# Kernel optimization log

Measured on AMD Instinct MI355X. Metric: run time of the kernel, lower is better.

The kernel has to match this reference:

```python
import jax, jax.numpy as jnp
import numpy as np

DIM = 2048
NUM_HEADS = 16
NUM_KV_HEADS = 4
HEAD_DIM = DIM // NUM_HEADS
GROUP = NUM_HEADS // NUM_KV_HEADS
ROPE_THETA = 10000.0
EPS = 1e-6


def setup_inputs() -> dict:
    key = jax.random.key(0)
    ks = jax.random.split(key, 6)
    B, L = 2, 2048
    x = jax.random.normal(ks[0], (B, L, DIM), dtype=jnp.float32)
    mask = jnp.ones((B, L), dtype=jnp.int32)
    s = 1.0 / np.sqrt(DIM)
    Wq = jax.random.normal(ks[1], (DIM, DIM), dtype=jnp.float32) * s
    Wk = jax.random.normal(ks[2], (NUM_KV_HEADS * HEAD_DIM, DIM), dtype=jnp.float32) * s
    Wv = jax.random.normal(ks[3], (NUM_KV_HEADS * HEAD_DIM, DIM), dtype=jnp.float32) * s
    Wo = jax.random.normal(ks[4], (DIM, DIM), dtype=jnp.float32) * s
    q_gamma = jnp.ones((HEAD_DIM,), dtype=jnp.float32)
    k_gamma = jnp.ones((HEAD_DIM,), dtype=jnp.float32)
    return {"x": x, "mask": mask, "Wq": Wq, "Wk": Wk, "Wv": Wv, "Wo": Wo,
            "q_gamma": q_gamma, "k_gamma": k_gamma}


def _rmsnorm(x, gamma):
    # normalize over last dim (head_dim)
    var = jnp.mean(jnp.square(x), axis=-1, keepdims=True)
    return x * jax.lax.rsqrt(var + EPS) * gamma


def _rope_cos_sin(L):
    inv_freq = 1.0 / (ROPE_THETA ** (jnp.arange(0, HEAD_DIM, 2, dtype=jnp.float32) / HEAD_DIM))
    t = jnp.arange(L, dtype=jnp.float32)
    freqs = jnp.outer(t, inv_freq)  # [L, hd/2]
    return jnp.cos(freqs), jnp.sin(freqs)


def _apply_rotary(x, cos, sin):
    # x: [B, H, L, hd]; rotate consecutive pairs (complex mul)
    xr = x.reshape(*x.shape[:-1], HEAD_DIM // 2, 2)
    re, im = xr[..., 0], xr[..., 1]
    c = cos[None, None, :, :]
    s = sin[None, None, :, :]
    out_re = re * c - im * s
    out_im = re * s + im * c
    return jnp.stack([out_re, out_im], axis=-1).reshape(x.shape)


def reference(x, mask, Wq, Wk, Wv, Wo, q_gamma, k_gamma):
    B, L, D = x.shape
    q = (x @ Wq.T).reshape(B, L, NUM_HEADS, HEAD_DIM)
    k = (x @ Wk.T).reshape(B, L, NUM_KV_HEADS, HEAD_DIM)
    v = (x @ Wv.T).reshape(B, L, NUM_KV_HEADS, HEAD_DIM)
    q = _rmsnorm(q, q_gamma)
    k = _rmsnorm(k, k_gamma)
    q = q.transpose(0, 2, 1, 3)  # [B, H, L, hd]
    k = k.transpose(0, 2, 1, 3)  # [B, Hkv, L, hd]
    v = v.transpose(0, 2, 1, 3)
    cos, sin = _rope_cos_sin(L)
    q = _apply_rotary(q, cos, sin)
    k = _apply_rotary(k, cos, sin)
    # repeat_interleave kv heads to match query heads
    k = jnp.repeat(k, GROUP, axis=1)
    v = jnp.repeat(v, GROUP, axis=1)
    scores = jnp.einsum('bhqd,bhkd->bhqk', q, k) / jnp.sqrt(jnp.float32(HEAD_DIM))
    m = mask[:, None, None, :]  # [B,1,1,L] padding mask
    scores = jnp.where(m == 0, -jnp.inf, scores)
    attn = jax.nn.softmax(scores.astype(jnp.float32), axis=-1).astype(scores.dtype)
    out = jnp.einsum('bhqk,bhkd->bhqd', attn, v)
    out = out.transpose(0, 2, 1, 3).reshape(B, L, NUM_HEADS * HEAD_DIM)
    return out @ Wo.T
```

## Files before the change

### kernel.cpp

```cpp
#include <hip/hip_runtime.h>
#include <hip/hip_bf16.h>
#include <stdint.h>

#define DIMN   2048
#define L_SEQ  2048
#define BATCH  2
#define NHEADS 16
#define NKVH   4
#define HDIM   128
#define MROWS  (BATCH * L_SEQ)
#define NQKV   (DIMN + 2 * NKVH * HDIM)

typedef unsigned short u16;
typedef __bf16 bf16_t;
typedef bf16_t bf16x8 __attribute__((ext_vector_type(8)));
typedef float  f32x4  __attribute__((ext_vector_type(4)));
typedef float  f32x16 __attribute__((ext_vector_type(16)));
typedef u16    u16x8  __attribute__((ext_vector_type(8)));

__device__ __forceinline__ u16 f2bf(float f) {
  union { float f; uint32_t u; } v; v.f = f;
  uint32_t r = v.u + 0x7fffu + ((v.u >> 16) & 1u);
  return (u16)(r >> 16);
}

__device__ __forceinline__ float fexp2(float x) {
  float r; asm("v_exp_f32 %0, %1" : "=v"(r) : "v"(x)); return r;
}
__device__ __forceinline__ uint32_t cvtpk(float a, float b) {
  uint32_t r; asm("v_cvt_pk_bf16_f32 %0, %1, %2" : "=v"(r) : "v"(a), "v"(b)); return r;
}
__device__ __forceinline__ void plswap(uint32_t& a, uint32_t& b) {
  asm volatile("v_permlane32_swap_b32 %0, %1" : "+v"(a), "+v"(b));
}

#define GLOAD_LDS16(gp, lp)                                                     \
  __builtin_amdgcn_global_load_lds(                                             \
      (const __attribute__((address_space(1))) void*)(gp),                      \
      (__attribute__((address_space(3))) void*)(lp), 16, 0, 0)

__global__ void conv_f32_bf16(const float* __restrict__ src,
                              u16* __restrict__ dst, int n4) {
  int i = blockIdx.x * blockDim.x + threadIdx.x;
  int stride = gridDim.x * blockDim.x;
  for (; i < n4; i += stride) {
    float4 v = ((const float4*)src)[i];
    ushort4 o;
    o.x = f2bf(v.x); o.y = f2bf(v.y); o.z = f2bf(v.z); o.w = f2bf(v.w);
    ((ushort4*)dst)[i] = o;
  }
}

__global__ __launch_bounds__(256) void gemm_bf16_bt(
    const u16* __restrict__ A, const u16* __restrict__ B,
    float* __restrict__ C, int M, int N, int K) {
  __shared__ u16 As[128 * 64];
  __shared__ u16 Bs[128 * 64];
  const int tid  = threadIdx.x;
  const int lane = tid & 63;
  const int wid  = tid >> 6;
  const int l15  = lane & 15, l4 = lane >> 4;
  const int bm = blockIdx.y, bn = blockIdx.x;
  const int wr = wid >> 1, wc = wid & 1;

  f32x4 acc[4][4] = {};

  for (int k0 = 0; k0 < K; k0 += 64) {
#pragma unroll
    for (int is = 0; is < 4; ++is) {
      int cc = is * 256 + tid;
      int rr = cc >> 3, c = (cc & 7) << 3;
      GLOAD_LDS16(A + (size_t)(bm * 128 + rr) * K + k0 + c,
                  &As[(is * 256 + wid * 64) * 8]);
      GLOAD_LDS16(B + (size_t)(bn * 128 + rr) * K + k0 + c,
                  &Bs[(is * 256 + wid * 64) * 8]);
    }
    __syncthreads();

#pragma unroll
    for (int kk = 0; kk < 2; ++kk) {
      const int ko = kk * 32 + l4 * 8;
      bf16x8 af[4], bfr[4];
#pragma unroll
      for (int m = 0; m < 4; ++m)
        af[m] = *(const bf16x8*)&As[(wr * 64 + m * 16 + l15) * 64 + ko];
#pragma unroll
      for (int n = 0; n < 4; ++n)
        bfr[n] = *(const bf16x8*)&Bs[(wc * 64 + n * 16 + l15) * 64 + ko];
#pragma unroll
      for (int m = 0; m < 4; ++m)
#pragma unroll
        for (int n = 0; n < 4; ++n)
          acc[m][n] = __builtin_amdgcn_mfma_f32_16x16x32_bf16(
              af[m], bfr[n], acc[m][n], 0, 0, 0);
    }
    __syncthreads();
  }

  const int crow0 = bm * 128 + wr * 64;
  const int ccol0 = bn * 128 + wc * 64;
#pragma unroll
  for (int m = 0; m < 4; ++m)
#pragma unroll
    for (int n = 0; n < 4; ++n)
#pragma unroll
      for (int j = 0; j < 4; ++j)
        C[(size_t)(crow0 + m * 16 + l4 * 4 + j) * N + ccol0 + n * 16 + l15] =
            acc[m][n][j];
}

#define QK_PRE 0.12751743f
__global__ __launch_bounds__(256) void rms_rope(
    const float* __restrict__ qkv, const float* __restrict__ qg,
    const float* __restrict__ kg, u16* __restrict__ qb,
    u16* __restrict__ kb) {
  const int gw   = blockIdx.x * 4 + (threadIdx.x >> 6);
  const int lane = threadIdx.x & 63;
  const int row  = gw / 20;
  const int slot = gw % 20;
  const int b = row >> 11, pos = row & 2047;

  int colbase = (slot < 16) ? slot * 128 : 2048 + (slot - 16) * 128;
  const float* src = qkv + (size_t)row * NQKV + colbase;
  float2 v = *(const float2*)(src + 2 * lane);
  float re = v.x, im = v.y;

  float ss = re * re + im * im;
#pragma unroll
  for (int m = 1; m < 64; m <<= 1) ss += __shfl_xor(ss, m, 64);
  float inv = rsqrtf(ss * (1.0f / 128.0f) + 1e-6f);
  const float* gamma = (slot < 16) ? qg : kg;
  re = re * inv * gamma[2 * lane];
  im = im * inv * gamma[2 * lane + 1];
  float freq = fexp2(-(float)lane * (13.287712379549449f / 64.0f));
  float ang = (float)pos * freq;
  float s, c;
  sincosf(ang, &s, &c);
  float ore = re * c - im * s;
  float oim = re * s + im * c;
  if (slot < 16) { ore *= QK_PRE; oim *= QK_PRE; }

  ushort2 o; o.x = f2bf(ore); o.y = f2bf(oim);
  u16* dst = (slot < 16)
      ? qb + ((size_t)((b * NHEADS + slot) * L_SEQ) + pos) * HDIM + 2 * lane
      : kb + ((size_t)((b * NKVH + slot - 16) * L_SEQ) + pos) * HDIM + 2 * lane;
  *(ushort2*)dst = o;
}

__global__ __launch_bounds__(256) void transpose_v(
    const float* __restrict__ qkv, u16* __restrict__ vt) {
  __shared__ u16 Ls[64][68];
  const int pt = blockIdx.x;
  const int dt = blockIdx.y;
  const int b  = blockIdx.z;
  const int t  = threadIdx.x;
  {
    int r0 = t >> 4;
    int c4 = (t & 15) << 2;
#pragma unroll
    for (int i = 0; i < 4; ++i) {
      int row = i * 16 + r0;
      float4 v = *(const float4*)(qkv + (size_t)(b * 2048 + pt * 64 + row) * NQKV
                                  + 2560 + dt * 64 + c4);
      Ls[row][c4 + 0] = f2bf(v.x); Ls[row][c4 + 1] = f2bf(v.y);
      Ls[row][c4 + 2] = f2bf(v.z); Ls[row][c4 + 3] = f2bf(v.w);
    }
  }
  __syncthreads();
#pragma unroll
  for (int it = 0; it < 2; ++it) {
    int slot = it * 256 + t;
    int dr = slot >> 3, ch = slot & 7;
    u16x8 o;
#pragma unroll
    for (int j = 0; j < 8; ++j) o[j] = Ls[ch * 8 + j][dr];
    int vc = dt * 64 + dr;
    int kvh = vc >> 7, dd = vc & 127;
    *(u16x8*)(vt + ((size_t)(b * NKVH + kvh) * HDIM + dd) * L_SEQ + pt * 64 + ch * 8) = o;
  }
}

__global__ __launch_bounds__(512) void attn_kernel(
    const u16* __restrict__ qb, const u16* __restrict__ kb,
    const u16* __restrict__ vt, const int* __restrict__ mask,
    u16* __restrict__ ob) {
  __shared__ u16 Ks[2][64 * 128];
  __shared__ u16 Vs[2][128 * 64];

  const int tid = threadIdx.x;
  const int lane = tid & 63, wid = tid >> 6;
  const int l31 = lane & 31, hi = lane >> 5;
  const int qt = blockIdx.x;
  const int bh = blockIdx.y;
  const int b = bh >> 4, h = bh & 15, kvh = h >> 2;

  const u16* Q  = qb + ((size_t)((b * NHEADS + h) * L_SEQ) + qt * 256 + wid * 32) * HDIM;
  const u16* Kg = kb + (size_t)((b * NKVH + kvh) * L_SEQ) * HDIM;
  const u16* Vg = vt + (size_t)((b * NKVH + kvh) * HDIM) * L_SEQ;
  const int* msk = mask + b * L_SEQ;

  bf16x8 qf[8];
  {
    const u16* qrow = Q + l31 * HDIM + hi * 8;
#pragma unroll
    for (int ds = 0; ds < 8; ++ds) qf[ds] = *(const bf16x8*)(qrow + ds * 16);
  }

  f32x16 o[4] = {};
  float m_run = -1e30f, l_run = 0.f;

#define STAGE(buf, tt)                                                          \
  {                                                                             \
    const int kv0 = (tt) * 64;                                                  \
    _Pragma("unroll")                                                           \
    for (int it = 0; it < 2; ++it) {                                            \
      int cc = it * 512 + tid;                                                  \
      int kr = cc >> 4, cs = cc & 15;                                           \
      GLOAD_LDS16(Kg + (size_t)(kv0 + kr) * HDIM + ((cs ^ (kr & 7)) << 3),      \
                  &Ks[buf][(it * 512 + wid * 64) * 8]);                         \
    }                                                                           \
    _Pragma("unroll")                                                           \
    for (int it = 0; it < 2; ++it) {                                            \
      int cc = it * 512 + tid;                                                  \
      int dr = cc >> 3, cs = cc & 7;                                            \
      GLOAD_LDS16(Vg + (size_t)dr * L_SEQ + kv0 + ((cs ^ (dr & 7)) << 3),       \
                  &Vs[buf][(it * 512 + wid * 64) * 8]);                         \
    }                                                                           \
  }

  STAGE(0, 0);
  __syncthreads();

  const int NT = L_SEQ / 64;
  for (int t = 0; t < NT; ++t) {
    const int cur = t & 1;
    if (t + 1 < NT) STAGE(cur ^ 1, t + 1);

    f32x16 st[2] = {};
#pragma unroll
    for (int s = 0; s < 2; ++s) {
      const int r = s * 32 + l31;
      const int rsw = r & 7;
#pragma unroll
      for (int ds = 0; ds < 8; ++ds) {
        bf16x8 kf = *(const bf16x8*)&Ks[cur][r * 128 + (((ds * 2 + hi) ^ rsw) << 3)];
        st[s] = __builtin_amdgcn_mfma_f32_32x32x16_bf16(kf, qf[ds], st[s], 0, 0, 0);
      }
    }

    int mk = msk[t * 64 + lane];
    if (!__all(mk != 0)) {
#pragma unroll
      for (int s = 0; s < 2; ++s)
#pragma unroll
        for (int r = 0; r < 16; ++r) {
          int k = t * 64 + s * 32 + (r & 3) + 8 * (r >> 2) + 4 * hi;
          if (msk[k] == 0) st[s][r] = -1e30f;
        }
    }

    float mx = st[0][0];
#pragma unroll
    for (int s = 0; s < 2; ++s)
#pragma unroll
      for (int r = 0; r < 16; ++r) mx = fmaxf(mx, st[s][r]);
    mx = fmaxf(mx, __shfl_xor(mx, 32, 64));

    if (!__all(mx <= m_run + 11.0f)) {
      float mn = fmaxf(m_run, mx);
      float alpha = fexp2(m_run - mn);
      m_run = mn;
      l_run *= alpha;
#pragma unroll
      for (int db = 0; db < 4; ++db)
#pragma unroll
        for (int r = 0; r < 16; ++r) o[db][r] *= alpha;
    }

    float psum = 0.f;
#pragma unroll
    for (int s = 0; s < 2; ++s)
#pragma unroll
      for (int r = 0; r < 16; ++r) {
        float p = fexp2(st[s][r] - m_run);
        psum += p;
        st[s][r] = p;
      }
    psum += __shfl_xor(psum, 32, 64);
    l_run += psum;

    bf16x8 pfrag[4];
#pragma unroll
    for (int s = 0; s < 2; ++s) {
      uint32_t Ap[4], Bp[4];
#pragma unroll
      for (int g = 0; g < 4; ++g) {
        Ap[g] = cvtpk(st[s][4 * g + 0], st[s][4 * g + 1]);
        Bp[g] = cvtpk(st[s][4 * g + 2], st[s][4 * g + 3]);
      }
#pragma unroll
      for (int kq = 0; kq < 2; ++kq) {
        uint32_t x0 = Ap[2 * kq], y0 = Ap[2 * kq + 1]; plswap(x0, y0);
        uint32_t x1 = Bp[2 * kq], y1 = Bp[2 * kq + 1]; plswap(x1, y1);
        union { uint32_t w[4]; bf16x8 v; } u;
        u.w[0] = x0; u.w[1] = x1; u.w[2] = y0; u.w[3] = y1;
        pfrag[s * 2 + kq] = u.v;
      }
    }

#pragma unroll
    for (int ks = 0; ks < 4; ++ks) {
#pragma unroll
      for (int db = 0; db < 4; ++db) {
        const int dr = db * 32 + l31;
        bf16x8 vf = *(const bf16x8*)&Vs[cur][dr * 64 + (((ks * 2 + hi) ^ (dr & 7)) << 3)];
        o[db] = __builtin_amdgcn_mfma_f32_32x32x16_bf16(vf, pfrag[ks], o[db], 0, 0, 0);
      }
    }

    __syncthreads();
  }

  float inv = 1.0f / l_run;
  u16* orow = ob + (size_t)(b * L_SEQ + qt * 256 + wid * 32 + l31) * DIMN + h * HDIM;
#pragma unroll
  for (int db = 0; db < 4; ++db)
#pragma unroll
    for (int r = 0; r < 16; r += 2) {
      int d = db * 32 + (r & 3) + 8 * (r >> 2) + 4 * hi;
      ushort2 o2;
      o2.x = f2bf(o[db][r] * inv);
      o2.y = f2bf(o[db][r + 1] * inv);
      *(ushort2*)(orow + d) = o2;
    }
}

extern "C" void kernel_launch(void* const* d_in, const int* in_sizes, int n_in,
                              void* d_out, int out_size, void* d_ws, size_t ws_size,
                              hipStream_t stream) {
  const float* x  = (const float*)d_in[0];
  const int* mask = (const int*)d_in[1];
  const float* Wq = (const float*)d_in[2];
  const float* Wk = (const float*)d_in[3];
  const float* Wv = (const float*)d_in[4];
  const float* Wo = (const float*)d_in[5];
  const float* qg = (const float*)d_in[6];
  const float* kg = (const float*)d_in[7];
  float* out = (float*)d_out;

  char* ws = (char*)d_ws;
  u16*   xb   = (u16*)(ws + 0);
  u16*   wqkv = (u16*)(ws + 16777216);
  u16*   wob  = (u16*)(ws + 29360128);
  float* qkv  = (float*)(ws + 37748736);
  u16*   qb   = (u16*)(ws + 88080384);
  u16*   kb   = (u16*)(ws + 104857600);
  u16*   vtb  = (u16*)(ws + 109051904);
  u16*   ob   = (u16*)(ws + 37748736);

  conv_f32_bf16<<<1024, 256, 0, stream>>>(x,  xb,   2097152);
  conv_f32_bf16<<<1024, 256, 0, stream>>>(Wq, wqkv, 1048576);
  conv_f32_bf16<<<512,  256, 0, stream>>>(Wk, wqkv + 4194304, 262144);
  conv_f32_bf16<<<512,  256, 0, stream>>>(Wv, wqkv + 5242880, 262144);
  conv_f32_bf16<<<1024, 256, 0, stream>>>(Wo, wob,  1048576);

  gemm_bf16_bt<<<dim3(NQKV / 128, MROWS / 128), 256, 0, stream>>>(
      xb, wqkv, qkv, MROWS, NQKV, DIMN);
  rms_rope<<<MROWS * 20 / 4, 256, 0, stream>>>(qkv, qg, kg, qb, kb);
  transpose_v<<<dim3(32, 8, 2), 256, 0, stream>>>(qkv, vtb);
  attn_kernel<<<dim3(L_SEQ / 256, BATCH * NHEADS), 512, 0, stream>>>(
      qb, kb, vtb, mask, ob);
  gemm_bf16_bt<<<dim3(DIMN / 128, MROWS / 128), 256, 0, stream>>>(
      ob, wob, out, MROWS, DIMN, DIMN);
}
```

Before: 372.5 us.

## Replace GEMM with 256x256-tile, multi-stage pipelined, swizzled-LDS kernel

Replaces the simple 128x128 bf16 GEMM, which used a single LDS buffer with a sync per k-step, with a 256x256-tile kernel using 512 threads. It uses an 8-slot LDS ring (128KB dynamic shared memory) with global_load_lds prefetch several half-steps ahead, XOR-swizzled LDS layout to avoid bank conflicts, explicit waitcnt/barrier scheduling and setprio around MFMA bursts. The goal is to overlap global loads with MFMA work and raise arithmetic intensity for both the QKV and output projections. Larger tiles reduce grid size (12x16 and 8x16 blocks), which may underfill the 256 CUs, and the heavy LDS use limits occupancy.

Result: no change. 366.3 us (-1.7%).

```diff
diff --git a/kernel.cpp b/kernel.cpp
--- a/kernel.cpp
+++ b/kernel.cpp
@@ -38,6 +38,12 @@
   __builtin_amdgcn_global_load_lds(                                             \
       (const __attribute__((address_space(1))) void*)(gp),                      \
       (__attribute__((address_space(3))) void*)(lp), 16, 0, 0)
+
+#define BARR   __builtin_amdgcn_s_barrier()
+#define SCHED0 __builtin_amdgcn_sched_barrier(0)
+#define LGKM0  asm volatile("s_waitcnt lgkmcnt(0)" ::: "memory")
+#define VMC4   asm volatile("s_waitcnt vmcnt(4)" ::: "memory")
+#define VMC0   asm volatile("s_waitcnt vmcnt(0)" ::: "memory")
 
 __global__ void conv_f32_bf16(const float* __restrict__ src,
                               u16* __restrict__ dst, int n4) {
@@ -51,62 +57,108 @@
   }
 }
 
-__global__ __launch_bounds__(256) void gemm_bf16_bt(
+__global__ __launch_bounds__(512, 2) void gemm256(
     const u16* __restrict__ A, const u16* __restrict__ B,
     float* __restrict__ C, int M, int N, int K) {
-  __shared__ u16 As[128 * 64];
-  __shared__ u16 Bs[128 * 64];
-  const int tid  = threadIdx.x;
-  const int lane = tid & 63;
-  const int wid  = tid >> 6;
-  const int l15  = lane & 15, l4 = lane >> 4;
+  extern __shared__ u16 lds[];
+  const int tid = threadIdx.x;
+  const int lane = tid & 63, wid = tid >> 6;
+  const int l15 = lane & 15, l4 = lane >> 4;
+  const int wm = wid >> 2, wn = wid & 3;
   const int bm = blockIdx.y, bn = blockIdx.x;
-  const int wr = wid >> 1, wc = wid & 1;
-
-  f32x4 acc[4][4] = {};
-
-  for (int k0 = 0; k0 < K; k0 += 64) {
-#pragma unroll
-    for (int is = 0; is < 4; ++is) {
-      int cc = is * 256 + tid;
-      int rr = cc >> 3, c = (cc & 7) << 3;
-      GLOAD_LDS16(A + (size_t)(bm * 128 + rr) * K + k0 + c,
-                  &As[(is * 256 + wid * 64) * 8]);
-      GLOAD_LDS16(B + (size_t)(bn * 128 + rr) * K + k0 + c,
-                  &Bs[(is * 256 + wid * 64) * 8]);
-    }
-    __syncthreads();
-
-#pragma unroll
-    for (int kk = 0; kk < 2; ++kk) {
-      const int ko = kk * 32 + l4 * 8;
-      bf16x8 af[4], bfr[4];
-#pragma unroll
-      for (int m = 0; m < 4; ++m)
-        af[m] = *(const bf16x8*)&As[(wr * 64 + m * 16 + l15) * 64 + ko];
-#pragma unroll
-      for (int n = 0; n < 4; ++n)
-        bfr[n] = *(const bf16x8*)&Bs[(wc * 64 + n * 16 + l15) * 64 + ko];
-#pragma unroll
-      for (int m = 0; m < 4; ++m)
-#pragma unroll
-        for (int n = 0; n < 4; ++n)
-          acc[m][n] = __builtin_amdgcn_mfma_f32_16x16x32_bf16(
-              af[m], bfr[n], acc[m][n], 0, 0, 0);
-    }
-    __syncthreads();
-  }
-
-  const int crow0 = bm * 128 + wr * 64;
-  const int ccol0 = bn * 128 + wc * 64;
-#pragma unroll
-  for (int m = 0; m < 4; ++m)
-#pragma unroll
-    for (int n = 0; n < 4; ++n)
+  const int rbA = bm * 256, rbB = bn * 256;
+  const int NKT = K >> 6;
+  const int swz = l4 ^ ((l15 ^ (l15 >> 2)) & 3);
+
+  f32x4 acc[8][4] = {};
+
+#define STAGE_U(h_)                                                            \
+  if ((h_) < 4 * NKT) {                                                        \
+    const int u_ = (h_) & 3;                                                   \
+    const u16* sp_ = (u_ & 1) ? B : A;                                         \
+    const int rb_ = (u_ & 1) ? rbB : rbA;                                      \
+    const int k0_ = (((h_) >> 2) << 6) + ((u_ >> 1) << 5);                     \
+    u16* dp_ = lds + (((h_) & 7) << 13) + (wid << 9);                          \
+    _Pragma("unroll")                                                          \
+    for (int i_ = 0; i_ < 2; ++i_) {                                           \
+      int cc_ = i_ * 512 + tid;                                                \
+      int r_ = cc_ >> 2;                                                       \
+      GLOAD_LDS16(sp_ + (size_t)(rb_ + r_) * K + k0_ +                         \
+                      (((cc_ & 3) ^ ((r_ ^ (r_ >> 2)) & 3)) << 3),             \
+                  dp_ + i_ * 4096);                                            \
+    }                                                                          \
+  }
+
+#define RD_A(dst, sA, rowbase)                                                 \
+  _Pragma("unroll")                                                            \
+  for (int mf_ = 0; mf_ < 4; ++mf_)                                            \
+    dst[mf_] = *(const bf16x8*)&lds[((sA) << 13) +                             \
+        ((rowbase) + mf_ * 16 + l15) * 32 + (swz << 3)];
+
+#define RD_B(dst, sB)                                                          \
+  _Pragma("unroll")                                                            \
+  for (int nf_ = 0; nf_ < 4; ++nf_)                                            \
+    dst[nf_] = *(const bf16x8*)&lds[((sB) << 13) +                             \
+        (wn * 64 + nf_ * 16 + l15) * 32 + (swz << 3)];
+
+#define MM(jj, aa, bb)                                                         \
+  __builtin_amdgcn_s_setprio(1);                                               \
+  _Pragma("unroll")                                                            \
+  for (int mf_ = 0; mf_ < 4; ++mf_)                                            \
+    _Pragma("unroll")                                                          \
+    for (int nf_ = 0; nf_ < 4; ++nf_)                                          \
+      acc[(jj) * 4 + mf_][nf_] = __builtin_amdgcn_mfma_f32_16x16x32_bf16(      \
+          aa[mf_], bb[nf_], acc[(jj) * 4 + mf_][nf_], 0, 0, 0);                \
+  __builtin_amdgcn_s_setprio(0);
+
+#pragma unroll
+  for (int h = 0; h < 6; ++h) { STAGE_U(h); }
+  VMC4;
+  BARR; SCHED0;
+
+  for (int c = 0; c < NKT; ++c) {
+    const int cb = (c & 1) << 2;
+    const int p0 = c << 2;
+    bf16x8 a[4], b[4];
+    RD_A(a, cb + 0, wm * 128);
+    RD_B(b, cb + 1);
+    STAGE_U(p0 + 6);
+    BARR; LGKM0; SCHED0;
+    MM(0, a, b);
+    BARR; SCHED0;
+    RD_A(a, cb + 0, wm * 128 + 64);
+    STAGE_U(p0 + 7);
+    BARR; LGKM0; SCHED0;
+    MM(1, a, b);
+    BARR; SCHED0;
+    RD_A(a, cb + 2, wm * 128);
+    RD_B(b, cb + 3);
+    STAGE_U(p0 + 8);
+    BARR; LGKM0; SCHED0;
+    MM(0, a, b);
+    BARR; SCHED0;
+    RD_A(a, cb + 2, wm * 128 + 64);
+    STAGE_U(p0 + 9);
+    BARR; LGKM0; SCHED0;
+    MM(1, a, b);
+    if (c == NKT - 2) { VMC0; } else if (c < NKT - 2) { VMC4; }
+    BARR; SCHED0;
+  }
+
+  const int crow0 = bm * 256 + wm * 128;
+  const int ccol0 = bn * 256 + wn * 64;
+#pragma unroll
+  for (int mf = 0; mf < 8; ++mf)
+#pragma unroll
+    for (int nf = 0; nf < 4; ++nf)
 #pragma unroll
       for (int j = 0; j < 4; ++j)
-        C[(size_t)(crow0 + m * 16 + l4 * 4 + j) * N + ccol0 + n * 16 + l15] =
-            acc[m][n][j];
+        C[(size_t)(crow0 + mf * 16 + l4 * 4 + j) * N + ccol0 + nf * 16 + l15] =
+            acc[mf][nf][j];
+#undef STAGE_U
+#undef RD_A
+#undef RD_B
+#undef MM
 }
 
 #define QK_PRE 0.12751743f
@@ -348,6 +400,9 @@
   const float* kg = (const float*)d_in[7];
   float* out = (float*)d_out;
 
+  hipFuncSetAttribute((const void*)gemm256,
+                      hipFuncAttributeMaxDynamicSharedMemorySize, 131072);
+
   char* ws = (char*)d_ws;
   u16*   xb   = (u16*)(ws + 0);
   u16*   wqkv = (u16*)(ws + 16777216);
@@ -364,12 +419,12 @@
   conv_f32_bf16<<<512,  256, 0, stream>>>(Wv, wqkv + 5242880, 262144);
   conv_f32_bf16<<<1024, 256, 0, stream>>>(Wo, wob,  1048576);
 
-  gemm_bf16_bt<<<dim3(NQKV / 128, MROWS / 128), 256, 0, stream>>>(
+  gemm256<<<dim3(NQKV / 256, MROWS / 256), 512, 131072, stream>>>(
       xb, wqkv, qkv, MROWS, NQKV, DIMN);
   rms_rope<<<MROWS * 20 / 4, 256, 0, stream>>>(qkv, qg, kg, qb, kb);
   transpose_v<<<dim3(32, 8, 2), 256, 0, stream>>>(qkv, vtb);
   attn_kernel<<<dim3(L_SEQ / 256, BATCH * NHEADS), 512, 0, stream>>>(
       qb, kb, vtb, mask, ob);
-  gemm_bf16_bt<<<dim3(DIMN / 128, MROWS / 128), 256, 0, stream>>>(
+  gemm256<<<dim3(DIMN / 256, MROWS / 256), 512, 131072, stream>>>(
       ob, wob, out, MROWS, DIMN, DIMN);
 }
```
